# Optimization experiments

Hardware: AMD Instinct MI355X
Metric: run time of the kernel (lower is better)

The kernel has to match this reference:

```python
import jax, jax.numpy as jnp
import numpy as np

NQ = 4
DIM = 1 << NQ  # 16 statevector amplitudes

def _cnot_perm(c, t):
    idx = np.arange(DIM)
    cbit = (idx >> (NQ - 1 - c)) & 1
    return np.where(cbit == 1, idx ^ (1 << (NQ - 1 - t)), idx)

# BasicEntanglerLayers CNOT ring: (0,1),(1,2),(2,3),(3,0)
CNOT_PERMS = [jnp.asarray(_cnot_perm(q, (q + 1) % NQ)) for q in range(NQ)]
_idx = np.arange(DIM)
SIGNS = jnp.asarray(np.stack([1.0 - 2.0 * ((_idx >> (NQ - 1 - q)) & 1) for q in range(NQ)]).astype(np.float32))  # (NQ, DIM), PauliZ eigenvalues


def _apply_rx(state, theta, q):
    """Apply RX(theta) on wire q. state: (N, DIM) complex64. theta: scalar or (N,)."""
    half = theta * 0.5
    c = jnp.cos(half).astype(jnp.complex64)
    js = (1j * jnp.sin(half)).astype(jnp.complex64)
    if jnp.ndim(theta) == 1:
        c = c[:, None, None]
        js = js[:, None, None]
    d1, d2 = 1 << q, 1 << (NQ - 1 - q)
    st = state.reshape(-1, d1, 2, d2)
    a0, a1 = st[:, :, 0, :], st[:, :, 1, :]
    out = jnp.stack([c * a0 - js * a1, c * a1 - js * a0], axis=2)
    return out.reshape(state.shape)


def circuit(angles, weights):
    """AngleEmbedding(RX) + BasicEntanglerLayers(RX + CNOT ring) + <Z_i>.
    angles: (N, NQ) real. weights: (L, NQ). returns (N, NQ)."""
    N = angles.shape[0]
    state = jnp.zeros((N, DIM), jnp.complex64).at[:, 0].set(1.0)
    for q in range(NQ):  # AngleEmbedding: per-sample RX angles
        state = _apply_rx(state, angles[:, q], q)
    for l in range(weights.shape[0]):  # entangler layers (static count)
        for q in range(NQ):
            state = _apply_rx(state, weights[l, q], q)
        for q in range(NQ):
            state = state[:, CNOT_PERMS[q]]
    probs = jnp.real(state) ** 2 + jnp.imag(state) ** 2
    return probs @ SIGNS.T


def setup_inputs() -> dict:
    key = jax.random.key(0)
    ks = jax.random.split(key, 5)
    B, S = 32, 2048
    TWO_PI = 6.2831853
    return {
        "x": jax.random.normal(ks[0], (B, S, NQ), jnp.float32),
        "weights_Q": jax.random.uniform(ks[1], (1, NQ), jnp.float32) * TWO_PI,
        "weights_K": jax.random.uniform(ks[2], (1, NQ), jnp.float32) * TWO_PI,
        "weights_V": jax.random.uniform(ks[3], (1, NQ), jnp.float32) * TWO_PI,
        "weights_C": jax.random.uniform(ks[4], (1, NQ), jnp.float32) * TWO_PI,
    }


def reference(x, weights_Q, weights_K, weights_V, weights_C):
    B, S, E = x.shape  # E == NQ == 4
    flat = x.reshape(B * S, E)
    Q = circuit(flat, weights_Q).reshape(B, S, E)
    K = circuit(flat, weights_K).reshape(B, S, E)
    V = circuit(flat, weights_V).reshape(B, S, E)
    scores = jnp.einsum('bqe,bke->bqk', Q, K) / (E ** 0.5)
    attn = jax.nn.softmax(scores, axis=-1)
    ctx = jnp.einsum('bqk,bke->bqe', attn, V)
    return circuit(ctx.reshape(B * S, E), weights_C).reshape(B, S, E)
```

## Files before the change

kernel.cpp:

```cpp
#include <hip/hip_runtime.h>

#define DIM 16
#define SEQ 2048
#define CHUNK 512
#define NCHUNK 4


template<int P>
__device__ __forceinline__ void rx_bit(float sr[DIM], float si[DIM], float ch, float sh) {
    constexpr int m = 1 << P;
    #pragma unroll
    for (int i = 0; i < DIM; ++i) {
        if ((i & m) == 0) {
            const int j = i | m;
            float r0 = sr[i], i0 = si[i], r1 = sr[j], i1 = si[j];
            sr[i] = fmaf(ch, r0,  sh * i1);
            si[i] = fmaf(ch, i0, -sh * r1);
            sr[j] = fmaf(ch, r1,  sh * i0);
            si[j] = fmaf(ch, i1, -sh * r0);
        }
    }
}

template<int PC, int PT>
__device__ __forceinline__ void cnot_g(float sr[DIM], float si[DIM]) {
    constexpr int cm = 1 << PC, tm = 1 << PT;
    #pragma unroll
    for (int i = 0; i < DIM; ++i) {
        if ((i & cm) && !(i & tm)) {
            const int j = i | tm;
            float t;
            t = sr[i]; sr[i] = sr[j]; sr[j] = t;
            t = si[i]; si[i] = si[j]; si[j] = t;
        }
    }
}

__device__ __forceinline__ void embed(float sr[DIM], float si[DIM], float4 a) {
    #pragma unroll
    for (int i = 0; i < DIM; ++i) { sr[i] = 0.f; si[i] = 0.f; }
    sr[0] = 1.f;
    float ch, sh;
    __sincosf(0.5f * a.x, &sh, &ch); rx_bit<3>(sr, si, ch, sh);
    __sincosf(0.5f * a.y, &sh, &ch); rx_bit<2>(sr, si, ch, sh);
    __sincosf(0.5f * a.z, &sh, &ch); rx_bit<1>(sr, si, ch, sh);
    __sincosf(0.5f * a.w, &sh, &ch); rx_bit<0>(sr, si, ch, sh);
}

__device__ __forceinline__ void layer(float sr[DIM], float si[DIM], float4 w) {
    float ch, sh;
    __sincosf(0.5f * w.x, &sh, &ch); rx_bit<3>(sr, si, ch, sh);
    __sincosf(0.5f * w.y, &sh, &ch); rx_bit<2>(sr, si, ch, sh);
    __sincosf(0.5f * w.z, &sh, &ch); rx_bit<1>(sr, si, ch, sh);
    __sincosf(0.5f * w.w, &sh, &ch); rx_bit<0>(sr, si, ch, sh);
    cnot_g<3,2>(sr, si);
    cnot_g<2,1>(sr, si);
    cnot_g<1,0>(sr, si);
    cnot_g<0,3>(sr, si);
}

__device__ __forceinline__ float4 measure(const float sr[DIM], const float si[DIM]) {
    float e0 = 0.f, e1 = 0.f, e2 = 0.f, e3 = 0.f;
    #pragma unroll
    for (int i = 0; i < DIM; ++i) {
        float p = fmaf(sr[i], sr[i], si[i] * si[i]);
        e0 += (i & 8) ? -p : p;
        e1 += (i & 4) ? -p : p;
        e2 += (i & 2) ? -p : p;
        e3 += (i & 1) ? -p : p;
    }
    return make_float4(e0, e1, e2, e3);
}


__global__ __launch_bounds__(256) void qkv_kernel(
        const float* __restrict__ x,
        const float* __restrict__ wQp, const float* __restrict__ wKp,
        const float* __restrict__ wVp,
        float4* __restrict__ Q, float4* __restrict__ KV) {
    const int i = blockIdx.x * 256 + threadIdx.x;
    const int which = blockIdx.y;
    const float4 xv = ((const float4*)x)[i];
    const float* wp = (which == 0) ? wQp : (which == 1) ? wKp : wVp;
    const float4 w = *(const float4*)wp;

    float sr[DIM], si[DIM];
    embed(sr, si, xv);
    layer(sr, si, w);
    const float4 r = measure(sr, si);

    if (which == 0)      Q[i]          = r;
    else if (which == 1) KV[2 * i]     = r;
    else                 KV[2 * i + 1] = r;
}


__global__ __launch_bounds__(256) void attn_partial(
        const float4* __restrict__ Q, const float4* __restrict__ KV,
        float* __restrict__ pden, float4* __restrict__ pctx, int n) {
    __shared__ float4 kvs[2 * CHUNK];

    const int rg = blockIdx.x;
    const int c  = blockIdx.y;
    const int b  = rg >> 3;

    const float4* src = KV + (size_t)b * (2 * SEQ) + c * (2 * CHUNK);
    for (int t = threadIdx.x; t < 2 * CHUNK; t += 256)
        kvs[t] = src[t];
    __syncthreads();

    const int row = rg * 256 + threadIdx.x;
    const float4 q = Q[row];
    const float SC = 0.72134752044f;
    const float qx = q.x * SC, qy = q.y * SC, qz = q.z * SC, qw = q.w * SC;

    float den = 0.f, a0 = 0.f, a1 = 0.f, a2 = 0.f, a3 = 0.f;
    #pragma unroll 8
    for (int k = 0; k < CHUNK; ++k) {
        const float4 kv = kvs[2 * k];
        const float4 vv = kvs[2 * k + 1];
        float s = fmaf(qx, kv.x, fmaf(qy, kv.y, fmaf(qz, kv.z, qw * kv.w)));
        float e = exp2f(s);
        den += e;
        a0 = fmaf(e, vv.x, a0);
        a1 = fmaf(e, vv.y, a1);
        a2 = fmaf(e, vv.z, a2);
        a3 = fmaf(e, vv.w, a3);
    }

    pden[c * n + row] = den;
    pctx[c * n + row] = make_float4(a0, a1, a2, a3);
}


__global__ __launch_bounds__(256) void combine_kernel(
        const float* __restrict__ pden, const float4* __restrict__ pctx,
        const float* __restrict__ wCp, float4* __restrict__ out, int n) {
    const int row = blockIdx.x * 256 + threadIdx.x;

    float d = 0.f;
    float c0 = 0.f, c1 = 0.f, c2 = 0.f, c3 = 0.f;
    #pragma unroll
    for (int c = 0; c < NCHUNK; ++c) {
        d += pden[c * n + row];
        const float4 p = pctx[c * n + row];
        c0 += p.x; c1 += p.y; c2 += p.z; c3 += p.w;
    }
    const float inv = 1.0f / d;
    const float4 ctx = make_float4(c0 * inv, c1 * inv, c2 * inv, c3 * inv);

    const float4 wC = *(const float4*)wCp;
    float sr[DIM], si[DIM];
    embed(sr, si, ctx);
    layer(sr, si, wC);
    out[row] = measure(sr, si);
}


extern "C" void kernel_launch(void* const* d_in, const int* in_sizes, int n_in,
                              void* d_out, int out_size, void* d_ws, size_t ws_size,
                              hipStream_t stream) {
    const float* x  = (const float*)d_in[0];
    const float* wQ = (const float*)d_in[1];
    const float* wK = (const float*)d_in[2];
    const float* wV = (const float*)d_in[3];
    const float* wC = (const float*)d_in[4];

    const int n = in_sizes[0] / 4;
    float4* Q    = (float4*)d_ws;
    float4* KV   = Q + n;
    float4* pctx = KV + 2 * n;
    float*  pden = (float*)(pctx + 4 * n);

    dim3 qgrid(n / 256, 3);
    qkv_kernel<<<qgrid, 256, 0, stream>>>(x, wQ, wK, wV, Q, KV);

    dim3 agrid(n / 256, NCHUNK);
    attn_partial<<<agrid, 256, 0, stream>>>(Q, KV, pden, pctx, n);

    combine_kernel<<<n / 256, 256, 0, stream>>>(pden, pctx, wC, (float4*)d_out, n);
}
```

Before: 123.4 us.

## Register-block four query rows per thread with packed FMA and raw exp2

Each thread in the attention partial kernel now handles four query rows, so every K/V value read from LDS is reused four times. The inner math uses 2-wide float vectors so the compiler can emit packed FMA instructions, and it calls the hardware exp2 builtin directly. Chunk size drops to 256 and the chunk count rises to 8 to keep the grid large, which doubles the partial-result traffic the combine step must read. Register pressure rises from the per-row accumulators.

```diff
diff --git a/kernel.cpp b/kernel.cpp
--- a/kernel.cpp
+++ b/kernel.cpp
@@ -2,8 +2,19 @@
 
 #define DIM 16
 #define SEQ 2048
-#define CHUNK 512
-#define NCHUNK 4
+#define CHUNK 256
+#define NCHUNK 8
+#define RPT 4
+
+typedef float v2f __attribute__((ext_vector_type(2)));
+
+static __device__ __forceinline__ float fexp2(float x) {
+#if __has_builtin(__builtin_amdgcn_exp2f)
+    return __builtin_amdgcn_exp2f(x);
+#else
+    return exp2f(x);
+#endif
+}
 
 
 template<int P>
@@ -102,34 +113,56 @@
 
     const int rg = blockIdx.x;
     const int c  = blockIdx.y;
-    const int b  = rg >> 3;
+    const int b  = rg >> 1;
 
     const float4* src = KV + (size_t)b * (2 * SEQ) + c * (2 * CHUNK);
     for (int t = threadIdx.x; t < 2 * CHUNK; t += 256)
         kvs[t] = src[t];
     __syncthreads();
 
-    const int row = rg * 256 + threadIdx.x;
-    const float4 q = Q[row];
     const float SC = 0.72134752044f;
-    const float qx = q.x * SC, qy = q.y * SC, qz = q.z * SC, qw = q.w * SC;
-
-    float den = 0.f, a0 = 0.f, a1 = 0.f, a2 = 0.f, a3 = 0.f;
-    #pragma unroll 8
+    const int row0 = rg * (256 * RPT) + threadIdx.x;
+
+    v2f qa[RPT], qb[RPT];
+    #pragma unroll
+    for (int j = 0; j < RPT; ++j) {
+        const float4 q = Q[row0 + j * 256];
+        qa[j] = (v2f){q.x * SC, q.y * SC};
+        qb[j] = (v2f){q.z * SC, q.w * SC};
+    }
+
+    float den[RPT];
+    v2f a01[RPT], a23[RPT];
+    #pragma unroll
+    for (int j = 0; j < RPT; ++j) {
+        den[j] = 0.f;
+        a01[j] = (v2f){0.f, 0.f};
+        a23[j] = (v2f){0.f, 0.f};
+    }
+
+    #pragma unroll 4
     for (int k = 0; k < CHUNK; ++k) {
         const float4 kv = kvs[2 * k];
         const float4 vv = kvs[2 * k + 1];
-        float s = fmaf(qx, kv.x, fmaf(qy, kv.y, fmaf(qz, kv.z, qw * kv.w)));
-        float e = exp2f(s);
-        den += e;
-        a0 = fmaf(e, vv.x, a0);
-        a1 = fmaf(e, vv.y, a1);
-        a2 = fmaf(e, vv.z, a2);
-        a3 = fmaf(e, vv.w, a3);
-    }
-
-    pden[c * n + row] = den;
-    pctx[c * n + row] = make_float4(a0, a1, a2, a3);
+        const v2f ka = (v2f){kv.x, kv.y}, kb = (v2f){kv.z, kv.w};
+        const v2f va = (v2f){vv.x, vv.y}, vb = (v2f){vv.z, vv.w};
+        #pragma unroll
+        for (int j = 0; j < RPT; ++j) {
+            v2f t = __builtin_elementwise_fma(qb[j], kb, qa[j] * ka);
+            float e = fexp2(t.x + t.y);
+            v2f e2 = (v2f){e, e};
+            a01[j] = __builtin_elementwise_fma(e2, va, a01[j]);
+            a23[j] = __builtin_elementwise_fma(e2, vb, a23[j]);
+            den[j] += e;
+        }
+    }
+
+    #pragma unroll
+    for (int j = 0; j < RPT; ++j) {
+        const int row = row0 + j * 256;
+        pden[c * n + row] = den[j];
+        pctx[c * n + row] = make_float4(a01[j].x, a01[j].y, a23[j].x, a23[j].y);
+    }
 }
 
 
@@ -170,12 +203,12 @@
     float4* Q    = (float4*)d_ws;
     float4* KV   = Q + n;
     float4* pctx = KV + 2 * n;
-    float*  pden = (float*)(pctx + 4 * n);
+    float*  pden = (float*)(pctx + NCHUNK * n);
 
     dim3 qgrid(n / 256, 3);
     qkv_kernel<<<qgrid, 256, 0, stream>>>(x, wQ, wK, wV, Q, KV);
 
-    dim3 agrid(n / 256, NCHUNK);
+    dim3 agrid(n / (256 * RPT), NCHUNK);
     attn_partial<<<agrid, 256, 0, stream>>>(Q, KV, pden, pctx, n);
 
     combine_kernel<<<n / 256, 256, 0, stream>>>(pden, pctx, wC, (float4*)d_out, n);
```

New measurement: 104.7 us. -15.2%, faster.
